# Kernel tuning notes

Measured on AMD Instinct MI355X. Metric: run time of the kernel, lower is better.

Reference implementation:

```python
import jax, jax.numpy as jnp
import numpy as np

B, L = 4, 2048
D_MODEL = 64          # d_model = input_size
ED = 128              # d_inner = expand_factor * d_model = hidden_size
N = 32                # d_state
DCONV = 16            # d_conv
NLAYERS = 4
DTRANK = 4            # ceil(d_model/16)
NCLS = 1
EPS = 1e-5


def setup_inputs() -> dict:
    key = jax.random.key(0)
    ks = jax.random.split(key, 10)
    g = lambda k, s, sc: jax.random.normal(k, s, dtype=jnp.float32) * sc
    inp = {}
    inp["x"] = jax.random.normal(ks[0], (B, L, D_MODEL), dtype=jnp.float32)
    inp["in_w"] = g(ks[1], (NLAYERS, 2 * ED, D_MODEL), 0.1)
    inp["in_b"] = jnp.zeros((NLAYERS, 2 * ED), jnp.float32)
    inp["conv_w"] = g(ks[2], (NLAYERS, ED, 1, DCONV), 0.1)  # depthwise kernel (OIH per group)
    inp["conv_b"] = jnp.zeros((NLAYERS, ED), jnp.float32)
    inp["xproj_w"] = g(ks[3], (NLAYERS, DTRANK + 2 * N, ED), 0.1)
    inp["dtproj_w"] = g(ks[4], (NLAYERS, ED, DTRANK), 0.5)
    inp["dtproj_b"] = g(ks[5], (NLAYERS, ED), 0.5)
    # S4D-real init: A[e, n] = n+1
    A = jnp.tile(jnp.arange(1, N + 1, dtype=jnp.float32), (ED, 1))
    inp["A_log"] = jnp.tile(jnp.log(A)[None], (NLAYERS, 1, 1))
    inp["Dp"] = jnp.ones((NLAYERS, ED), jnp.float32)
    inp["outproj_w"] = g(ks[6], (NLAYERS, D_MODEL, ED), 0.1)
    inp["outproj_b"] = jnp.zeros((NLAYERS, D_MODEL), jnp.float32)
    inp["norm_w"] = jnp.ones((NLAYERS, D_MODEL), jnp.float32)
    inp["fc_w"] = g(ks[7], (NCLS, ED), 0.1)
    inp["fc_b"] = jnp.zeros((NCLS,), jnp.float32)
    return inp


def _rmsnorm(x, w):
    return x * jax.lax.rsqrt(jnp.mean(x * x, axis=-1, keepdims=True) + EPS) * w


def _causal_dwconv(x, w, b):
    # x: [B,L,ED], w: [ED,1,DCONV] depthwise, causal left pad
    xt = jnp.swapaxes(x, 1, 2)  # [B,ED,L]
    y = jax.lax.conv_general_dilated(
        xt, w, window_strides=(1,), padding=[(DCONV - 1, 0)],
        dimension_numbers=("NCH", "OIH", "NCH"), feature_group_count=ED)
    return jnp.swapaxes(y, 1, 2) + b


def _mamba_block(h, in_w, in_b, conv_w, conv_b, xproj_w, dtproj_w, dtproj_b,
                 A_log, Dp, outproj_w, outproj_b, last):
    xz = jnp.einsum("bld,ed->ble", h, in_w) + in_b          # [B,L,2ED]
    xin, z = jnp.split(xz, 2, axis=-1)
    xc = jax.nn.silu(_causal_dwconv(xin, conv_w, conv_b))    # [B,L,ED]
    dbc = jnp.einsum("ble,re->blr", xc, xproj_w)             # [B,L,DTRANK+2N]
    delta = dbc[..., :DTRANK]
    Bm = dbc[..., DTRANK:DTRANK + N]                          # [B,L,N]
    Cm = dbc[..., DTRANK + N:]                                # [B,L,N]
    delta = jax.nn.softplus(jnp.einsum("blr,er->ble", delta, dtproj_w) + dtproj_b)
    A = -jnp.exp(A_log)                                       # [ED,N]
    dA = jnp.exp(delta[..., None] * A)                        # [B,L,ED,N]
    dBu = delta[..., None] * Bm[:, :, None, :] * xc[..., None]  # [B,L,ED,N]

    def step(hs, t):
        dA_t, dBu_t, C_t = t                                  # [B,ED,N],[B,ED,N],[B,N]
        hs = dA_t * hs + dBu_t
        y = jnp.einsum("ben,bn->be", hs, C_t)
        return hs, y

    h0 = jnp.zeros((xc.shape[0], ED, N), dtype=xc.dtype)
    _, ys = jax.lax.scan(step, h0, (jnp.swapaxes(dA, 0, 1),
                                    jnp.swapaxes(dBu, 0, 1),
                                    jnp.swapaxes(Cm, 0, 1)))
    y = jnp.swapaxes(ys, 0, 1) + Dp * xc                      # [B,L,ED]
    y = y * jax.nn.silu(z)
    if last:
        return y                                              # classifier taps d_inner features
    return jnp.einsum("ble,de->bld", y, outproj_w) + outproj_b


def reference(x, in_w, in_b, conv_w, conv_b, xproj_w, dtproj_w, dtproj_b,
              A_log, Dp, outproj_w, outproj_b, norm_w, fc_w, fc_b):
    h = x
    for i in range(NLAYERS - 1):
        h = h + _mamba_block(_rmsnorm(h, norm_w[i]), in_w[i], in_b[i], conv_w[i],
                             conv_b[i], xproj_w[i], dtproj_w[i], dtproj_b[i],
                             A_log[i], Dp[i], outproj_w[i], outproj_b[i], False)
    i = NLAYERS - 1
    y = _mamba_block(_rmsnorm(h, norm_w[i]), in_w[i], in_b[i], conv_w[i],
                     conv_b[i], xproj_w[i], dtproj_w[i], dtproj_b[i],
                     A_log[i], Dp[i], outproj_w[i], outproj_b[i], True)
    last_hidden = y[:, -1, :]                                 # [B,ED]
    return last_hidden @ fc_w.T + fc_b                        # [B,NCLS]
```

## Files before the change

### kernel.cpp

```cpp
#include <hip/hip_runtime.h>
#include <math.h>

#define BSZ 4
#define Lseq 2048
#define DM 64
#define ED 128
#define NST 32
#define DCONVK 16
#define NLAYERS 4
#define DTRANK 4
#define EPSV 1e-5f
#define NC 128
#define TT 16
#define NSEG 8
#define L2E 1.4426950408889634f

#if defined(__has_builtin)
#if __has_builtin(__builtin_amdgcn_exp2f)
#define EXP2F(x) __builtin_amdgcn_exp2f(x)
#else
#define EXP2F(x) exp2f(x)
#endif
#else
#define EXP2F(x) exp2f(x)
#endif

__device__ __forceinline__ float sigf(float x) { return 1.0f / (1.0f + __expf(-x)); }
__device__ __forceinline__ float hsum4(float4 a) { return (a.x + a.y) + (a.z + a.w); }

__device__ __forceinline__ void inproj16(
    const float* in_w_l, const float* in_b_l, const float (*hn)[DM],
    float* xin, float* zbuf, size_t t0, int tid)
{
    float4 w4[16];
    const float4* wr = (const float4*)(in_w_l + tid * DM);
    #pragma unroll
    for (int i = 0; i < 16; ++i) w4[i] = wr[i];
    const float bias = in_b_l[tid];
    #pragma unroll 2
    for (int tok = 0; tok < TT; ++tok) {
        const float4* hv4 = (const float4*)&hn[tok][0];
        float4 a4 = make_float4(0.f, 0.f, 0.f, 0.f);
        #pragma unroll
        for (int i = 0; i < 16; ++i) {
            float4 hv = hv4[i];
            a4.x = fmaf(hv.x, w4[i].x, a4.x);
            a4.y = fmaf(hv.y, w4[i].y, a4.y);
            a4.z = fmaf(hv.z, w4[i].z, a4.z);
            a4.w = fmaf(hv.w, w4[i].w, a4.w);
        }
        const float r = bias + hsum4(a4);
        if (tid < ED) xin[(t0 + tok) * ED + tid] = r;
        else          zbuf[(t0 + tok) * ED + (tid - ED)] = r;
    }
}

__global__ __launch_bounds__(256) void k_layer_gemm(
    const float* __restrict__ hin, const float* __restrict__ norm_w,
    const float* __restrict__ in_w, const float* __restrict__ in_b,
    float* __restrict__ xin, float* __restrict__ zb, float* __restrict__ out)
{
    const int t0 = blockIdx.x * TT;
    const int tid = threadIdx.x;
    const int lane = tid & 63;
    const int wv = tid >> 6;
    __shared__ __align__(16) float hn[TT][DM];

    if (blockIdx.x == 0 && tid < BSZ) out[tid] = 0.f;

    const float nw = norm_w[lane];
    float hval[4];
    #pragma unroll
    for (int j = 0; j < 4; ++j)
        hval[j] = hin[(size_t)(t0 + wv * 4 + j) * DM + lane];

    #pragma unroll
    for (int j = 0; j < 4; ++j) {
        float ss = hval[j] * hval[j];
        #pragma unroll
        for (int off = 32; off; off >>= 1) ss += __shfl_xor(ss, off, 64);
        const float sc = rsqrtf(ss * (1.0f / DM) + EPSV);
        hn[wv * 4 + j][lane] = hval[j] * sc * nw;
    }
    __syncthreads();
    inproj16(in_w, in_b, (const float (*)[DM])hn, xin, zb, (size_t)t0, tid);
}

__global__ __launch_bounds__(256) void k_conv_scan(
    const float* __restrict__ xin, const float* __restrict__ conv_w,
    const float* __restrict__ conv_b, const float* __restrict__ xproj_w,
    const float* __restrict__ dtproj_w, const float* __restrict__ dtproj_b,
    const float* __restrict__ A_log,
    float* __restrict__ xc_out, float* __restrict__ delta_out,
    float* __restrict__ Bout, float* __restrict__ Cout,
    float* __restrict__ dsum_out, float* __restrict__ hloc, int store_dbc)
{
    const int blk = blockIdx.x;
    const int b   = blk >> 7;
    const int c   = blk & 127;
    const int l0  = c * TT;
    const size_t t0 = (size_t)b * Lseq + l0;
    const int tid = threadIdx.x;
    const int e = tid & 127, half = tid >> 7;
    const bool doXC = store_dbc || (c == NC - 1);
    __shared__ __align__(16) float xs[(TT + DCONVK - 1) * ED];
    __shared__ __align__(16) float xcs[TT][ED];
    __shared__ __align__(16) float Bs[TT][NST];
    __shared__ float dts[TT][DTRANK];
    float (*dl)[ED] = (float (*)[ED])xs;

    float Aen16[16];
    {
        const float4* a4 = (const float4*)(A_log + e * NST + half * 16);
        #pragma unroll
        for (int i = 0; i < 4; ++i) {
            float4 v = a4[i];
            Aen16[i*4+0] = -__expf(v.x) * L2E; Aen16[i*4+1] = -__expf(v.y) * L2E;
            Aen16[i*4+2] = -__expf(v.z) * L2E; Aen16[i*4+3] = -__expf(v.w) * L2E;
        }
    }
    float w[DCONVK];
    {
        const float4* cw = (const float4*)(conv_w + e * DCONVK);
        #pragma unroll
        for (int i = 0; i < 4; ++i) {
            float4 cc = cw[i];
            w[i*4+0] = cc.x; w[i*4+1] = cc.y; w[i*4+2] = cc.z; w[i*4+3] = cc.w;
        }
    }
    const float cb = conv_b[e];

    {
        const int NV = (TT + DCONVK - 1) * ED / 4;
        for (int idx4 = tid; idx4 < NV; idx4 += 256) {
            const int row = idx4 >> 5;
            const int lrow = l0 - (DCONVK - 1) + row;
            float4 v = make_float4(0.f, 0.f, 0.f, 0.f);
            if (lrow >= 0)
                v = ((const float4*)(xin + ((size_t)b * Lseq + lrow) * ED))[idx4 & 31];
            ((float4*)xs)[idx4] = v;
        }
    }
    __syncthreads();

    {
        #pragma unroll 2
        for (int j = 0; j < 8; ++j) {
            const int tok = half * 8 + j;
            float acc = cb;
            #pragma unroll
            for (int k = 0; k < DCONVK; ++k)
                acc = fmaf(xs[(tok + k) * ED + e], w[k], acc);
            const float xcv = acc * sigf(acc);
            xcs[tok][e] = xcv;
            if (doXC) xc_out[(t0 + tok) * ED + e] = xcv;
        }
    }
    __syncthreads();

    {
        const int wv = tid >> 6, lane = tid & 63;
        float4 acc[4];
        #pragma unroll
        for (int j = 0; j < 4; ++j) acc[j] = make_float4(0.f, 0.f, 0.f, 0.f);
        #pragma unroll 1
        for (int p = 0; p < 4; ++p) {
            float4 w4[8];
            const float4* wr = (const float4*)(xproj_w + lane * ED + p * 32);
            #pragma unroll
            for (int i = 0; i < 8; ++i) w4[i] = wr[i];
            #pragma unroll
            for (int j = 0; j < 4; ++j) {
                const float4* yv = (const float4*)&xcs[wv * 4 + j][p * 32];
                #pragma unroll
                for (int i = 0; i < 8; ++i) {
                    float4 hv = yv[i];
                    acc[j].x = fmaf(hv.x, w4[i].x, acc[j].x);
                    acc[j].y = fmaf(hv.y, w4[i].y, acc[j].y);
                    acc[j].z = fmaf(hv.z, w4[i].z, acc[j].z);
                    acc[j].w = fmaf(hv.w, w4[i].w, acc[j].w);
                }
            }
        }
        #pragma unroll
        for (int j = 0; j < 4; ++j) {
            const int tok = wv * 4 + j;
            const float v = hsum4(acc[j]);
            if (lane < DTRANK) {
                dts[tok][lane] = v;
            } else if (lane < DTRANK + NST) {
                Bs[tok][lane - DTRANK] = v;
                if (store_dbc) Bout[(t0 + tok) * NST + (lane - DTRANK)] = v;
            } else {
                if (doXC) Cout[(t0 + tok) * NST + (lane - DTRANK - NST)] = v;
            }
        }
        {
            const int ridx = lane & 3;
            const int ks   = (lane >> 2) & 3;
            const int tsub = lane >> 4;
            const int r4   = 64 + ridx;
            const int tok  = wv * 4 + tsub;
            const float4* wr = (const float4*)(xproj_w + r4 * ED + ks * 32);
            const float4* yv = (const float4*)&xcs[tok][ks * 32];
            float4 a4 = make_float4(0.f, 0.f, 0.f, 0.f);
            #pragma unroll
            for (int i = 0; i < 8; ++i) {
                float4 hv = yv[i]; float4 wv4 = wr[i];
                a4.x = fmaf(hv.x, wv4.x, a4.x);
                a4.y = fmaf(hv.y, wv4.y, a4.y);
                a4.z = fmaf(hv.z, wv4.z, a4.z);
                a4.w = fmaf(hv.w, wv4.w, a4.w);
            }
            float v = hsum4(a4);
            v += __shfl_xor(v, 4, 64);
            v += __shfl_xor(v, 8, 64);
            if (ks == 0 && doXC) Cout[(t0 + tok) * NST + (r4 - DTRANK - NST)] = v;
        }
    }
    __syncthreads();

    {
        const float4 dwv = *(const float4*)(dtproj_w + e * DTRANK);
        const float bias = dtproj_b[e];
        #pragma unroll 2
        for (int j = 0; j < 8; ++j) {
            const int tok = half * 8 + j;
            float a = bias;
            a = fmaf(dts[tok][0], dwv.x, a);
            a = fmaf(dts[tok][1], dwv.y, a);
            a = fmaf(dts[tok][2], dwv.z, a);
            a = fmaf(dts[tok][3], dwv.w, a);
            const float sp = fmaxf(a, 0.f) + log1pf(__expf(-fabsf(a)));
            dl[tok][e] = sp;
            if (store_dbc) delta_out[(t0 + tok) * ED + e] = sp;
        }
    }
    __syncthreads();

    {
        float dsum = 0.f;
        #pragma unroll 4
        for (int l = 0; l < TT; ++l) dsum += dl[l][e];
        if (half == 0) dsum_out[((size_t)b * NC + c) * ED + e] = dsum;

        #pragma unroll 1
        for (int g = 0; g < 2; ++g) {
            const int n0 = half * 16 + g * 8;
            float Aen[8];
            #pragma unroll
            for (int k = 0; k < 8; ++k) Aen[k] = Aen16[g * 8 + k];
            float hs[8];
            #pragma unroll
            for (int k = 0; k < 8; ++k) hs[k] = 0.f;
            #pragma unroll 2
            for (int l = 0; l < TT; ++l) {
                const float de   = dl[l][e];
                const float dexc = de * xcs[l][e];
                const float4 B0 = *(const float4*)&Bs[l][n0];
                const float4 B1 = *(const float4*)&Bs[l][n0 + 4];
                float a;
                a = EXP2F(de * Aen[0]); hs[0] = fmaf(a, hs[0], B0.x * dexc);
                a = EXP2F(de * Aen[1]); hs[1] = fmaf(a, hs[1], B0.y * dexc);
                a = EXP2F(de * Aen[2]); hs[2] = fmaf(a, hs[2], B0.z * dexc);
                a = EXP2F(de * Aen[3]); hs[3] = fmaf(a, hs[3], B0.w * dexc);
                a = EXP2F(de * Aen[4]); hs[4] = fmaf(a, hs[4], B1.x * dexc);
                a = EXP2F(de * Aen[5]); hs[5] = fmaf(a, hs[5], B1.y * dexc);
                a = EXP2F(de * Aen[6]); hs[6] = fmaf(a, hs[6], B1.z * dexc);
                a = EXP2F(de * Aen[7]); hs[7] = fmaf(a, hs[7], B1.w * dexc);
            }
            const size_t idx = (((size_t)b * NC + c) * ED + e) * NST + n0;
            *(float4*)(hloc + idx)     = make_float4(hs[0], hs[1], hs[2], hs[3]);
            *(float4*)(hloc + idx + 4) = make_float4(hs[4], hs[5], hs[6], hs[7]);
        }
    }
}

__global__ __launch_bounds__(256) void k_scan_combine(
    const float* __restrict__ dsum, float* __restrict__ hloc,
    const float* __restrict__ A_log,
    const float* __restrict__ Cv, const float* __restrict__ xc,
    const float* __restrict__ zb, const float* __restrict__ Dp,
    const float* __restrict__ fcw, const float* __restrict__ fcb,
    float* __restrict__ out, int final)
{
    const int tid = threadIdx.x;
    const int tt  = tid & 31;
    const int seg = tid >> 5;
    const int t   = blockIdx.x * 32 + tt;
    const int b   = t >> 12;
    const int en  = t & 4095;
    const int e   = en >> 5;

    const float Aen2 = -__expf(A_log[en]) * L2E;

    const int c0 = seg * (NC / NSEG);
    const size_t idxBase = (size_t)b * NC * (ED * NST) + en;
    const size_t dBase   = (size_t)b * NC * ED + e;

    float u[NC / NSEG], a[NC / NSEG];
    #pragma unroll
    for (int k = 0; k < NC / NSEG; ++k)
        u[k] = hloc[idxBase + (size_t)(c0 + k) * (ED * NST)];
    #pragma unroll
    for (int k = 0; k < NC / NSEG; ++k)
        a[k] = EXP2F(Aen2 * dsum[dBase + (size_t)(c0 + k) * ED]);

    float A = 1.f, U = 0.f;
    #pragma unroll
    for (int k = 0; k < NC / NSEG; ++k) { U = fmaf(a[k], U, u[k]); A *= a[k]; }

    __shared__ float As[NSEG][32], Us[NSEG][32];
    As[seg][tt] = A; Us[seg][tt] = U;
    __syncthreads();

    float h = 0.f;
    #pragma unroll
    for (int j = 0; j < NSEG - 1; ++j)
        if (j < seg) h = fmaf(As[j][tt], h, Us[j][tt]);

    #pragma unroll
    for (int k = 0; k < NC / NSEG; ++k) {
        hloc[idxBase + (size_t)(c0 + k) * (ED * NST)] = h;
        h = fmaf(a[k], h, u[k]);
    }

    if (final && seg == NSEG - 1) {
        const int n = en & 31;
        const size_t tok = (size_t)b * Lseq + (Lseq - 1);
        float p = h * Cv[tok * NST + n];
        #pragma unroll
        for (int off = 16; off; off >>= 1) p += __shfl_xor(p, off, 32);
        if (n == 0) {
            const float xce = xc[tok * ED + e];
            const float zi  = zb[tok * ED + e];
            float val = (p + Dp[e] * xce) * (zi * sigf(zi)) * fcw[e];
            if (en == 0) val += fcb[0];
            atomicAdd(&out[b], val);
        }
    }
}

__global__ __launch_bounds__(256) void k_scan_gemm(
    const float* __restrict__ delta, const float* __restrict__ Bv,
    const float* __restrict__ Cv, const float* __restrict__ xc,
    const float* __restrict__ zbin, const float* __restrict__ A_log,
    const float* __restrict__ Dp, const float* __restrict__ hinit,
    const float* __restrict__ ow, const float* __restrict__ ob,
    const float* __restrict__ hin, const float* __restrict__ norm_w,
    const float* __restrict__ in_w, const float* __restrict__ in_b,
    float* __restrict__ hout, float* __restrict__ xin, float* __restrict__ zb)
{
    const int blk = blockIdx.x;
    const int b   = blk >> 7;
    const int c   = blk & 127;
    const int l0  = c * TT;
    const size_t t0 = (size_t)b * Lseq + l0;
    const int tid = threadIdx.x;
    const int e = tid & 127, half = tid >> 7;

    __shared__ __align__(16) float dlS[TT][ED];
    __shared__ __align__(16) float xcS[TT][ED];
    __shared__ __align__(16) float BsS[TT][NST];
    __shared__ __align__(16) float CsS[TT][NST];
    __shared__ __align__(16) float ys[TT][ED];
    __shared__ __align__(16) float pp[2][TT][ED];
    __shared__ __align__(16) float hn[TT][DM];

    float Aen16[16];
    {
        const float4* a4 = (const float4*)(A_log + e * NST + half * 16);
        #pragma unroll
        for (int i = 0; i < 4; ++i) {
            float4 v = a4[i];
            Aen16[i*4+0] = -__expf(v.x) * L2E; Aen16[i*4+1] = -__expf(v.y) * L2E;
            Aen16[i*4+2] = -__expf(v.z) * L2E; Aen16[i*4+3] = -__expf(v.w) * L2E;
        }
    }

    {
        const float4* dsrc = (const float4*)(delta + t0 * ED);
        const float4* xsrc = (const float4*)(xc + t0 * ED);
        float4* ddst = (float4*)&dlS[0][0];
        float4* xdst = (float4*)&xcS[0][0];
        #pragma unroll
        for (int i = 0; i < 2; ++i) {
            ddst[tid + i * 256] = dsrc[tid + i * 256];
            xdst[tid + i * 256] = xsrc[tid + i * 256];
        }
        if (tid < 128) {
            ((float4*)&BsS[0][0])[tid] = ((const float4*)(Bv + t0 * NST))[tid];
            ((float4*)&CsS[0][0])[tid] = ((const float4*)(Cv + t0 * NST))[tid];
        }
    }
    __syncthreads();

    #pragma unroll 1
    for (int g = 0; g < 2; ++g) {
        const int n0 = half * 16 + g * 8;
        float Aen[8];
        #pragma unroll
        for (int k = 0; k < 8; ++k) Aen[k] = Aen16[g * 8 + k];
        float hs[8];
        {
            const size_t idx = (((size_t)b * NC + c) * ED + e) * NST + n0;
            const float4 h0 = *(const float4*)(hinit + idx);
            const float4 h1 = *(const float4*)(hinit + idx + 4);
            hs[0] = h0.x; hs[1] = h0.y; hs[2] = h0.z; hs[3] = h0.w;
            hs[4] = h1.x; hs[5] = h1.y; hs[6] = h1.z; hs[7] = h1.w;
        }
        #pragma unroll 2
        for (int l = 0; l < TT; ++l) {
            const float de   = dlS[l][e];
            const float dexc = de * xcS[l][e];
            const float4 B0 = *(const float4*)&BsS[l][n0];
            const float4 B1 = *(const float4*)&BsS[l][n0 + 4];
            const float4 C0 = *(const float4*)&CsS[l][n0];
            const float4 C1 = *(const float4*)&CsS[l][n0 + 4];
            float a, p = 0.f;
            a = EXP2F(de * Aen[0]); hs[0] = fmaf(a, hs[0], B0.x * dexc); p = fmaf(hs[0], C0.x, p);
            a = EXP2F(de * Aen[1]); hs[1] = fmaf(a, hs[1], B0.y * dexc); p = fmaf(hs[1], C0.y, p);
            a = EXP2F(de * Aen[2]); hs[2] = fmaf(a, hs[2], B0.z * dexc); p = fmaf(hs[2], C0.z, p);
            a = EXP2F(de * Aen[3]); hs[3] = fmaf(a, hs[3], B0.w * dexc); p = fmaf(hs[3], C0.w, p);
            a = EXP2F(de * Aen[4]); hs[4] = fmaf(a, hs[4], B1.x * dexc); p = fmaf(hs[4], C1.x, p);
            a = EXP2F(de * Aen[5]); hs[5] = fmaf(a, hs[5], B1.y * dexc); p = fmaf(hs[5], C1.y, p);
            a = EXP2F(de * Aen[6]); hs[6] = fmaf(a, hs[6], B1.z * dexc); p = fmaf(hs[6], C1.z, p);
            a = EXP2F(de * Aen[7]); hs[7] = fmaf(a, hs[7], B1.w * dexc); p = fmaf(hs[7], C1.w, p);
            if (g == 0) pp[half][l][e] = p;
            else        pp[half][l][e] += p;
        }
    }
    __syncthreads();
    {
        const float dpe = Dp[e];
        #pragma unroll 2
        for (int j = 0; j < 8; ++j) {
            const int tl = half * 8 + j;
            const size_t tok = t0 + tl;
            const float p = pp[0][tl][e] + pp[1][tl][e];
            const float zi = zbin[tok * ED + e];
            ys[tl][e] = (p + dpe * xcS[tl][e]) * (zi * sigf(zi));
        }
    }
    __syncthreads();

    const int lane = tid & 63;
    const int wv = tid >> 6;
    const float nw = norm_w[lane];
    float hval[4];
    {
        float4 acc[4];
        #pragma unroll
        for (int j = 0; j < 4; ++j) acc[j] = make_float4(0.f, 0.f, 0.f, 0.f);
        #pragma unroll 1
        for (int p = 0; p < 4; ++p) {
            float4 w4[8];
            const float4* wr = (const float4*)(ow + lane * ED + p * 32);
            #pragma unroll
            for (int q = 0; q < 8; ++q) w4[q] = wr[q];
            #pragma unroll
            for (int j = 0; j < 4; ++j) {
                const float4* yv = (const float4*)&ys[wv * 4 + j][p * 32];
                #pragma unroll
                for (int q = 0; q < 8; ++q) {
                    float4 hv = yv[q];
                    acc[j].x = fmaf(hv.x, w4[q].x, acc[j].x);
                    acc[j].y = fmaf(hv.y, w4[q].y, acc[j].y);
                    acc[j].z = fmaf(hv.z, w4[q].z, acc[j].z);
                    acc[j].w = fmaf(hv.w, w4[q].w, acc[j].w);
                }
            }
        }
        const float obd = ob[lane];
        #pragma unroll
        for (int j = 0; j < 4; ++j) {
            const size_t tok = t0 + wv * 4 + j;
            hval[j] = hsum4(acc[j]) + obd + hin[tok * DM + lane];
            hout[tok * DM + lane] = hval[j];
        }
    }
    #pragma unroll
    for (int j = 0; j < 4; ++j) {
        float ss = hval[j] * hval[j];
        #pragma unroll
        for (int off = 32; off; off >>= 1) ss += __shfl_xor(ss, off, 64);
        const float sc = rsqrtf(ss * (1.0f / DM) + EPSV);
        hn[wv * 4 + j][lane] = hval[j] * sc * nw;
    }
    __syncthreads();
    inproj16(in_w, in_b, (const float (*)[DM])hn, xin, zb, t0, tid);
}

extern "C" void kernel_launch(void* const* d_in, const int* in_sizes, int n_in,
                              void* d_out, int out_size, void* d_ws, size_t ws_size,
                              hipStream_t stream)
{
    const float* x         = (const float*)d_in[0];
    const float* in_w      = (const float*)d_in[1];
    const float* in_b      = (const float*)d_in[2];
    const float* conv_w    = (const float*)d_in[3];
    const float* conv_b    = (const float*)d_in[4];
    const float* xproj_w   = (const float*)d_in[5];
    const float* dtproj_w  = (const float*)d_in[6];
    const float* dtproj_b  = (const float*)d_in[7];
    const float* A_log     = (const float*)d_in[8];
    const float* Dp        = (const float*)d_in[9];
    const float* outproj_w = (const float*)d_in[10];
    const float* outproj_b = (const float*)d_in[11];
    const float* norm_w    = (const float*)d_in[12];
    const float* fc_w      = (const float*)d_in[13];
    const float* fc_b      = (const float*)d_in[14];

    const size_t TOK = (size_t)BSZ * Lseq;
    float* ws = (float*)d_ws;
    float* h0    = ws; ws += TOK * DM;
    float* h1    = ws; ws += TOK * DM;
    float* xin   = ws; ws += TOK * ED;
    float* zbuf  = ws; ws += TOK * ED;
    float* xc    = ws; ws += TOK * ED;
    float* dlt   = ws; ws += TOK * ED;
    float* Bv    = ws; ws += TOK * NST;
    float* Cv    = ws; ws += TOK * NST;
    float* dsum  = ws; ws += (size_t)BSZ * NC * ED;
    float* hloc  = ws; ws += (size_t)BSZ * NC * ED * NST;

    const float* hres = x;
    float* hbufs[2] = { h0, h1 };

    k_layer_gemm<<<(int)(TOK / TT), 256, 0, stream>>>(
        x, norm_w, in_w, in_b, xin, zbuf, (float*)d_out);

    for (int i = 0; i < NLAYERS; ++i) {
        const int last = (i == NLAYERS - 1);
        const float* Alog_i = A_log + (size_t)i * ED * NST;
        k_conv_scan<<<(int)(BSZ * NC), 256, 0, stream>>>(
            xin, conv_w + (size_t)i * ED * DCONVK, conv_b + (size_t)i * ED,
            xproj_w + (size_t)i * (DTRANK + 2 * NST) * ED,
            dtproj_w + (size_t)i * ED * DTRANK, dtproj_b + (size_t)i * ED,
            Alog_i, xc, dlt, Bv, Cv, dsum, hloc, last ? 0 : 1);
        k_scan_combine<<<(BSZ * ED * NST * NSEG) / 256, 256, 0, stream>>>(
            dsum, hloc, Alog_i, Cv, xc, zbuf, Dp + (size_t)i * ED,
            fc_w, fc_b, (float*)d_out, last ? 1 : 0);
        if (!last) {
            float* hout = hbufs[i & 1];
            k_scan_gemm<<<(int)(BSZ * NC), 256, 0, stream>>>(
                dlt, Bv, Cv, xc, zbuf, Alog_i, Dp + (size_t)i * ED, hloc,
                outproj_w + (size_t)i * DM * ED, outproj_b + (size_t)i * DM,
                hres, norm_w + (size_t)(i + 1) * DM,
                in_w + (size_t)(i + 1) * 2 * ED * DM,
                in_b + (size_t)(i + 1) * 2 * ED,
                hout, xin, zbuf);
            hres = hout;
        }
    }
}
```

Before: 308.1 us.

## Fuse all layer kernels into one persistent kernel with grid barriers

```diff
diff --git a/kernel.cpp b/kernel.cpp
--- a/kernel.cpp
+++ b/kernel.cpp
@@ -13,6 +13,7 @@
 #define NC 128
 #define TT 16
 #define NSEG 8
+#define GRIDN (BSZ * NC)
 #define L2E 1.4426950408889634f
 
 #if defined(__has_builtin)
@@ -27,6 +28,19 @@
 
 __device__ __forceinline__ float sigf(float x) { return 1.0f / (1.0f + __expf(-x)); }
 __device__ __forceinline__ float hsum4(float4 a) { return (a.x + a.y) + (a.z + a.w); }
+
+__device__ __forceinline__ void gbar(unsigned int* cnt, unsigned int target)
+{
+    __syncthreads();
+    if (threadIdx.x == 0) {
+        __threadfence();
+        __hip_atomic_fetch_add(cnt, 1u, __ATOMIC_RELEASE, __HIP_MEMORY_SCOPE_AGENT);
+        while (__hip_atomic_load(cnt, __ATOMIC_RELAXED, __HIP_MEMORY_SCOPE_AGENT) < target)
+            __builtin_amdgcn_s_sleep(1);
+        __threadfence();
+    }
+    __syncthreads();
+}
 
 __device__ __forceinline__ void inproj16(
     const float* in_w_l, const float* in_b_l, const float (*hn)[DM],
@@ -55,462 +69,452 @@
     }
 }
 
-__global__ __launch_bounds__(256) void k_layer_gemm(
-    const float* __restrict__ hin, const float* __restrict__ norm_w,
-    const float* __restrict__ in_w, const float* __restrict__ in_b,
-    float* __restrict__ xin, float* __restrict__ zb, float* __restrict__ out)
+struct KParams {
+    const float *x, *in_w, *in_b, *conv_w, *conv_b, *xproj_w, *dtproj_w,
+                *dtproj_b, *A_log, *Dp, *outproj_w, *outproj_b, *norm_w,
+                *fc_w, *fc_b;
+    float *out, *h0, *h1, *xin, *zbuf, *xc, *dlt, *Bv, *Cv, *dsum, *hloc;
+    unsigned int* bar;
+};
+
+__global__ __launch_bounds__(256, 2) void k_mamba(KParams P)
 {
-    const int t0 = blockIdx.x * TT;
+    const int bid = blockIdx.x;
     const int tid = threadIdx.x;
-    const int lane = tid & 63;
-    const int wv = tid >> 6;
-    __shared__ __align__(16) float hn[TT][DM];
-
-    if (blockIdx.x == 0 && tid < BSZ) out[tid] = 0.f;
-
-    const float nw = norm_w[lane];
-    float hval[4];
-    #pragma unroll
-    for (int j = 0; j < 4; ++j)
-        hval[j] = hin[(size_t)(t0 + wv * 4 + j) * DM + lane];
-
-    #pragma unroll
-    for (int j = 0; j < 4; ++j) {
-        float ss = hval[j] * hval[j];
+    unsigned int bk = 0;
+    __shared__ __align__(16) float smem[12288];
+
+    if (bid == 0 && tid < BSZ) P.out[tid] = 0.f;
+
+    {
+        float (*hn)[DM] = (float (*)[DM])smem;
+        const size_t t0 = (size_t)bid * TT;
+        const int lane = tid & 63, wv = tid >> 6;
+        const float nw = P.norm_w[lane];
+        float hval[4];
         #pragma unroll
-        for (int off = 32; off; off >>= 1) ss += __shfl_xor(ss, off, 64);
-        const float sc = rsqrtf(ss * (1.0f / DM) + EPSV);
-        hn[wv * 4 + j][lane] = hval[j] * sc * nw;
+        for (int j = 0; j < 4; ++j)
+            hval[j] = P.x[(t0 + wv * 4 + j) * DM + lane];
+        #pragma unroll
+        for (int j = 0; j < 4; ++j) {
+            float ss = hval[j] * hval[j];
+            #pragma unroll
+            for (int off = 32; off; off >>= 1) ss += __shfl_xor(ss, off, 64);
+            const float sc = rsqrtf(ss * (1.0f / DM) + EPSV);
+            hn[wv * 4 + j][lane] = hval[j] * sc * nw;
+        }
+        __syncthreads();
+        inproj16(P.in_w, P.in_b, (const float (*)[DM])hn, P.xin, P.zbuf, t0, tid);
     }
-    __syncthreads();
-    inproj16(in_w, in_b, (const float (*)[DM])hn, xin, zb, (size_t)t0, tid);
-}
-
-__global__ __launch_bounds__(256) void k_conv_scan(
-    const float* __restrict__ xin, const float* __restrict__ conv_w,
-    const float* __restrict__ conv_b, const float* __restrict__ xproj_w,
-    const float* __restrict__ dtproj_w, const float* __restrict__ dtproj_b,
-    const float* __restrict__ A_log,
-    float* __restrict__ xc_out, float* __restrict__ delta_out,
-    float* __restrict__ Bout, float* __restrict__ Cout,
-    float* __restrict__ dsum_out, float* __restrict__ hloc, int store_dbc)
-{
-    const int blk = blockIdx.x;
-    const int b   = blk >> 7;
-    const int c   = blk & 127;
-    const int l0  = c * TT;
-    const size_t t0 = (size_t)b * Lseq + l0;
-    const int tid = threadIdx.x;
-    const int e = tid & 127, half = tid >> 7;
-    const bool doXC = store_dbc || (c == NC - 1);
-    __shared__ __align__(16) float xs[(TT + DCONVK - 1) * ED];
-    __shared__ __align__(16) float xcs[TT][ED];
-    __shared__ __align__(16) float Bs[TT][NST];
-    __shared__ float dts[TT][DTRANK];
-    float (*dl)[ED] = (float (*)[ED])xs;
-
-    float Aen16[16];
-    {
-        const float4* a4 = (const float4*)(A_log + e * NST + half * 16);
-        #pragma unroll
-        for (int i = 0; i < 4; ++i) {
-            float4 v = a4[i];
-            Aen16[i*4+0] = -__expf(v.x) * L2E; Aen16[i*4+1] = -__expf(v.y) * L2E;
-            Aen16[i*4+2] = -__expf(v.z) * L2E; Aen16[i*4+3] = -__expf(v.w) * L2E;
+    gbar(P.bar, ++bk * GRIDN);
+
+    #pragma unroll 1
+    for (int li = 0; li < NLAYERS; ++li) {
+        const int last = (li == NLAYERS - 1);
+        const float* Alog = P.A_log + (size_t)li * ED * NST;
+        const float* Dpl  = P.Dp + (size_t)li * ED;
+
+        {
+            const int b = bid >> 7, c = bid & 127;
+            const int l0 = c * TT;
+            const size_t t0 = (size_t)b * Lseq + l0;
+            const int e = tid & 127, half = tid >> 7;
+            const int store_dbc = last ? 0 : 1;
+            const bool doXC = store_dbc || (c == NC - 1);
+
+            float* xs = smem;
+            float (*xcs)[ED] = (float (*)[ED])(smem + 4096);
+            float (*Bs)[NST] = (float (*)[NST])(smem + 6144);
+            float (*dts)[DTRANK] = (float (*)[DTRANK])(smem + 6656);
+            float (*dl)[ED] = (float (*)[ED])xs;
+
+            const float* conv_w   = P.conv_w + (size_t)li * ED * DCONVK;
+            const float* conv_b   = P.conv_b + (size_t)li * ED;
+            const float* xproj_w  = P.xproj_w + (size_t)li * (DTRANK + 2 * NST) * ED;
+            const float* dtproj_w = P.dtproj_w + (size_t)li * ED * DTRANK;
+            const float* dtproj_b = P.dtproj_b + (size_t)li * ED;
+
+            float Aen16[16];
+            {
+                const float4* a4 = (const float4*)(Alog + e * NST + half * 16);
+                #pragma unroll
+                for (int i = 0; i < 4; ++i) {
+                    float4 v = a4[i];
+                    Aen16[i*4+0] = -__expf(v.x) * L2E; Aen16[i*4+1] = -__expf(v.y) * L2E;
+                    Aen16[i*4+2] = -__expf(v.z) * L2E; Aen16[i*4+3] = -__expf(v.w) * L2E;
+                }
+            }
+            float w[DCONVK];
+            {
+                const float4* cw = (const float4*)(conv_w + e * DCONVK);
+                #pragma unroll
+                for (int i = 0; i < 4; ++i) {
+                    float4 cc = cw[i];
+                    w[i*4+0] = cc.x; w[i*4+1] = cc.y; w[i*4+2] = cc.z; w[i*4+3] = cc.w;
+                }
+            }
+            const float cb = conv_b[e];
+
+            {
+                const int NV = (TT + DCONVK - 1) * ED / 4;
+                for (int idx4 = tid; idx4 < NV; idx4 += 256) {
+                    const int row = idx4 >> 5;
+                    const int lrow = l0 - (DCONVK - 1) + row;
+                    float4 v = make_float4(0.f, 0.f, 0.f, 0.f);
+                    if (lrow >= 0)
+                        v = ((const float4*)(P.xin + ((size_t)b * Lseq + lrow) * ED))[idx4 & 31];
+                    ((float4*)xs)[idx4] = v;
+                }
+            }
+            __syncthreads();
+
+            {
+                #pragma unroll 2
+                for (int j = 0; j < 8; ++j) {
+                    const int tok = half * 8 + j;
+                    float acc = cb;
+                    #pragma unroll
+                    for (int k = 0; k < DCONVK; ++k)
+                        acc = fmaf(xs[(tok + k) * ED + e], w[k], acc);
+                    const float xcv = acc * sigf(acc);
+                    xcs[tok][e] = xcv;
+                    if (doXC) P.xc[(t0 + tok) * ED + e] = xcv;
+                }
+            }
+            __syncthreads();
+
+            {
+                const int wv = tid >> 6, lane = tid & 63;
+                float4 acc[4];
+                #pragma unroll
+                for (int j = 0; j < 4; ++j) acc[j] = make_float4(0.f, 0.f, 0.f, 0.f);
+                #pragma unroll 1
+                for (int p = 0; p < 4; ++p) {
+                    float4 w4[8];
+                    const float4* wr = (const float4*)(xproj_w + lane * ED + p * 32);
+                    #pragma unroll
+                    for (int i = 0; i < 8; ++i) w4[i] = wr[i];
+                    #pragma unroll
+                    for (int j = 0; j < 4; ++j) {
+                        const float4* yv = (const float4*)&xcs[wv * 4 + j][p * 32];
+                        #pragma unroll
+                        for (int i = 0; i < 8; ++i) {
+                            float4 hv = yv[i];
+                            acc[j].x = fmaf(hv.x, w4[i].x, acc[j].x);
+                            acc[j].y = fmaf(hv.y, w4[i].y, acc[j].y);
+                            acc[j].z = fmaf(hv.z, w4[i].z, acc[j].z);
+                            acc[j].w = fmaf(hv.w, w4[i].w, acc[j].w);
+                        }
+                    }
+                }
+                #pragma unroll
+                for (int j = 0; j < 4; ++j) {
+                    const int tok = wv * 4 + j;
+                    const float v = hsum4(acc[j]);
+                    if (lane < DTRANK) {
+                        dts[tok][lane] = v;
+                    } else if (lane < DTRANK + NST) {
+                        Bs[tok][lane - DTRANK] = v;
+                        if (store_dbc) P.Bv[(t0 + tok) * NST + (lane - DTRANK)] = v;
+                    } else {
+                        if (doXC) P.Cv[(t0 + tok) * NST + (lane - DTRANK - NST)] = v;
+                    }
+                }
+                {
+                    const int ridx = lane & 3;
+                    const int ks   = (lane >> 2) & 3;
+                    const int tsub = lane >> 4;
+                    const int r4   = 64 + ridx;
+                    const int tok  = wv * 4 + tsub;
+                    const float4* wr = (const float4*)(xproj_w + r4 * ED + ks * 32);
+                    const float4* yv = (const float4*)&xcs[tok][ks * 32];
+                    float4 a4 = make_float4(0.f, 0.f, 0.f, 0.f);
+                    #pragma unroll
+                    for (int i = 0; i < 8; ++i) {
+                        float4 hv = yv[i]; float4 wv4 = wr[i];
+                        a4.x = fmaf(hv.x, wv4.x, a4.x);
+                        a4.y = fmaf(hv.y, wv4.y, a4.y);
+                        a4.z = fmaf(hv.z, wv4.z, a4.z);
+                        a4.w = fmaf(hv.w, wv4.w, a4.w);
+                    }
+                    float v = hsum4(a4);
+                    v += __shfl_xor(v, 4, 64);
+                    v += __shfl_xor(v, 8, 64);
+                    if (ks == 0 && doXC) P.Cv[(t0 + tok) * NST + (r4 - DTRANK - NST)] = v;
+                }
+            }
+            __syncthreads();
+
+            {
+                const float4 dwv = *(const float4*)(dtproj_w + e * DTRANK);
+                const float bias = dtproj_b[e];
+                #pragma unroll 2
+                for (int j = 0; j < 8; ++j) {
+                    const int tok = half * 8 + j;
+                    float a = bias;
+                    a = fmaf(dts[tok][0], dwv.x, a);
+                    a = fmaf(dts[tok][1], dwv.y, a);
+                    a = fmaf(dts[tok][2], dwv.z, a);
+                    a = fmaf(dts[tok][3], dwv.w, a);
+                    const float sp = fmaxf(a, 0.f) + log1pf(__expf(-fabsf(a)));
+                    dl[tok][e] = sp;
+                    if (store_dbc) P.dlt[(t0 + tok) * ED + e] = sp;
+                }
+            }
+            __syncthreads();
+
+            {
+                float dsum = 0.f;
+                #pragma unroll 4
+                for (int l = 0; l < TT; ++l) dsum += dl[l][e];
+                if (half == 0) P.dsum[((size_t)b * NC + c) * ED + e] = dsum;
+
+                #pragma unroll 1
+                for (int g = 0; g < 2; ++g) {
+                    const int n0 = half * 16 + g * 8;
+                    float Aen[8];
+                    #pragma unroll
+                    for (int k = 0; k < 8; ++k) Aen[k] = Aen16[g * 8 + k];
+                    float hs[8];
+                    #pragma unroll
+                    for (int k = 0; k < 8; ++k) hs[k] = 0.f;
+                    #pragma unroll 2
+                    for (int l = 0; l < TT; ++l) {
+                        const float de   = dl[l][e];
+                        const float dexc = de * xcs[l][e];
+                        const float4 B0 = *(const float4*)&Bs[l][n0];
+                        const float4 B1 = *(const float4*)&Bs[l][n0 + 4];
+                        float a;
+                        a = EXP2F(de * Aen[0]); hs[0] = fmaf(a, hs[0], B0.x * dexc);
+                        a = EXP2F(de * Aen[1]); hs[1] = fmaf(a, hs[1], B0.y * dexc);
+                        a = EXP2F(de * Aen[2]); hs[2] = fmaf(a, hs[2], B0.z * dexc);
+                        a = EXP2F(de * Aen[3]); hs[3] = fmaf(a, hs[3], B0.w * dexc);
+                        a = EXP2F(de * Aen[4]); hs[4] = fmaf(a, hs[4], B1.x * dexc);
+                        a = EXP2F(de * Aen[5]); hs[5] = fmaf(a, hs[5], B1.y * dexc);
+                        a = EXP2F(de * Aen[6]); hs[6] = fmaf(a, hs[6], B1.z * dexc);
+                        a = EXP2F(de * Aen[7]); hs[7] = fmaf(a, hs[7], B1.w * dexc);
+                    }
+                    const size_t idx = (((size_t)b * NC + c) * ED + e) * NST + n0;
+                    *(float4*)(P.hloc + idx)     = make_float4(hs[0], hs[1], hs[2], hs[3]);
+                    *(float4*)(P.hloc + idx + 4) = make_float4(hs[4], hs[5], hs[6], hs[7]);
+                }
+            }
+        }
+        gbar(P.bar, ++bk * GRIDN);
+
+        {
+            const int tt  = tid & 31;
+            const int seg = tid >> 5;
+            const int t   = bid * 32 + tt;
+            const int b   = t >> 12;
+            const int en  = t & 4095;
+            const int e   = en >> 5;
+
+            const float Aen2 = -__expf(Alog[en]) * L2E;
+
+            const int c0 = seg * (NC / NSEG);
+            const size_t idxBase = (size_t)b * NC * (ED * NST) + en;
+            const size_t dBase   = (size_t)b * NC * ED + e;
+
+            float u[NC / NSEG], a[NC / NSEG];
+            #pragma unroll
+            for (int k = 0; k < NC / NSEG; ++k)
+                u[k] = P.hloc[idxBase + (size_t)(c0 + k) * (ED * NST)];
+            #pragma unroll
+            for (int k = 0; k < NC / NSEG; ++k)
+                a[k] = EXP2F(Aen2 * P.dsum[dBase + (size_t)(c0 + k) * ED]);
+
+            float A = 1.f, U = 0.f;
+            #pragma unroll
+            for (int k = 0; k < NC / NSEG; ++k) { U = fmaf(a[k], U, u[k]); A *= a[k]; }
+
+            float (*As)[32] = (float (*)[32])smem;
+            float (*Us)[32] = (float (*)[32])(smem + NSEG * 32);
+            As[seg][tt] = A; Us[seg][tt] = U;
+            __syncthreads();
+
+            float h = 0.f;
+            #pragma unroll
+            for (int j = 0; j < NSEG - 1; ++j)
+                if (j < seg) h = fmaf(As[j][tt], h, Us[j][tt]);
+
+            #pragma unroll
+            for (int k = 0; k < NC / NSEG; ++k) {
+                P.hloc[idxBase + (size_t)(c0 + k) * (ED * NST)] = h;
+                h = fmaf(a[k], h, u[k]);
+            }
+
+            if (last && seg == NSEG - 1) {
+                const int n = en & 31;
+                const size_t tok = (size_t)b * Lseq + (Lseq - 1);
+                float p = h * P.Cv[tok * NST + n];
+                #pragma unroll
+                for (int off = 16; off; off >>= 1) p += __shfl_xor(p, off, 32);
+                if (n == 0) {
+                    const float xce = P.xc[tok * ED + e];
+                    const float zi  = P.zbuf[tok * ED + e];
+                    float val = (p + Dpl[e] * xce) * (zi * sigf(zi)) * P.fc_w[e];
+                    if (en == 0) val += P.fc_b[0];
+                    atomicAdd(&P.out[b], val);
+                }
+            }
+        }
+
+        if (!last) {
+            gbar(P.bar, ++bk * GRIDN);
+            {
+                const int b = bid >> 7, c = bid & 127;
+                const int l0 = c * TT;
+                const size_t t0 = (size_t)b * Lseq + l0;
+                const int e = tid & 127, half = tid >> 7;
+
+                float (*dlS)[ED] = (float (*)[ED])(smem);
+                float (*xcS)[ED] = (float (*)[ED])(smem + 2048);
+                float (*BsS)[NST] = (float (*)[NST])(smem + 4096);
+                float (*CsS)[NST] = (float (*)[NST])(smem + 4608);
+                float (*ys)[ED]  = (float (*)[ED])(smem + 5120);
+                float (*pp)[TT][ED] = (float (*)[TT][ED])(smem + 7168);
+                float (*hn)[DM]  = (float (*)[DM])(smem + 11264);
+
+                const float* ow = P.outproj_w + (size_t)li * DM * ED;
+                const float* ob = P.outproj_b + (size_t)li * DM;
+                const float* hres = (li == 0) ? P.x : ((li == 1) ? P.h0 : P.h1);
+                float* hout = (li & 1) ? P.h1 : P.h0;
+
+                float Aen16[16];
+                {
+                    const float4* a4 = (const float4*)(Alog + e * NST + half * 16);
+                    #pragma unroll
+                    for (int i = 0; i < 4; ++i) {
+                        float4 v = a4[i];
+                        Aen16[i*4+0] = -__expf(v.x) * L2E; Aen16[i*4+1] = -__expf(v.y) * L2E;
+                        Aen16[i*4+2] = -__expf(v.z) * L2E; Aen16[i*4+3] = -__expf(v.w) * L2E;
+                    }
+                }
+
+                {
+                    const float4* dsrc = (const float4*)(P.dlt + t0 * ED);
+                    const float4* xsrc = (const float4*)(P.xc + t0 * ED);
+                    float4* ddst = (float4*)&dlS[0][0];
+                    float4* xdst = (float4*)&xcS[0][0];
+                    #pragma unroll
+                    for (int i = 0; i < 2; ++i) {
+                        ddst[tid + i * 256] = dsrc[tid + i * 256];
+                        xdst[tid + i * 256] = xsrc[tid + i * 256];
+                    }
+                    if (tid < 128) {
+                        ((float4*)&BsS[0][0])[tid] = ((const float4*)(P.Bv + t0 * NST))[tid];
+                        ((float4*)&CsS[0][0])[tid] = ((const float4*)(P.Cv + t0 * NST))[tid];
+                    }
+                }
+                __syncthreads();
+
+                #pragma unroll 1
+                for (int g = 0; g < 2; ++g) {
+                    const int n0 = half * 16 + g * 8;
+                    float Aen[8];
+                    #pragma unroll
+                    for (int k = 0; k < 8; ++k) Aen[k] = Aen16[g * 8 + k];
+                    float hs[8];
+                    {
+                        const size_t idx = (((size_t)b * NC + c) * ED + e) * NST + n0;
+                        const float4 h0v = *(const float4*)(P.hloc + idx);
+                        const float4 h1v = *(const float4*)(P.hloc + idx + 4);
+                        hs[0] = h0v.x; hs[1] = h0v.y; hs[2] = h0v.z; hs[3] = h0v.w;
+                        hs[4] = h1v.x; hs[5] = h1v.y; hs[6] = h1v.z; hs[7] = h1v.w;
+                    }
+                    #pragma unroll 2
+                    for (int l = 0; l < TT; ++l) {
+                        const float de   = dlS[l][e];
+                        const float dexc = de * xcS[l][e];
+                        const float4 B0 = *(const float4*)&BsS[l][n0];
+                        const float4 B1 = *(const float4*)&BsS[l][n0 + 4];
+                        const float4 C0 = *(const float4*)&CsS[l][n0];
+                        const float4 C1 = *(const float4*)&CsS[l][n0 + 4];
+                        float a, p = 0.f;
+                        a = EXP2F(de * Aen[0]); hs[0] = fmaf(a, hs[0], B0.x * dexc); p = fmaf(hs[0], C0.x, p);
+                        a = EXP2F(de * Aen[1]); hs[1] = fmaf(a, hs[1], B0.y * dexc); p = fmaf(hs[1], C0.y, p);
+                        a = EXP2F(de * Aen[2]); hs[2] = fmaf(a, hs[2], B0.z * dexc); p = fmaf(hs[2], C0.z, p);
+                        a = EXP2F(de * Aen[3]); hs[3] = fmaf(a, hs[3], B0.w * dexc); p = fmaf(hs[3], C0.w, p);
+                        a = EXP2F(de * Aen[4]); hs[4] = fmaf(a, hs[4], B1.x * dexc); p = fmaf(hs[4], C1.x, p);
+                        a = EXP2F(de * Aen[5]); hs[5] = fmaf(a, hs[5], B1.y * dexc); p = fmaf(hs[5], C1.y, p);
+                        a = EXP2F(de * Aen[6]); hs[6] = fmaf(a, hs[6], B1.z * dexc); p = fmaf(hs[6], C1.z, p);
+                        a = EXP2F(de * Aen[7]); hs[7] = fmaf(a, hs[7], B1.w * dexc); p = fmaf(hs[7], C1.w, p);
+                        if (g == 0) pp[half][l][e] = p;
+                        else        pp[half][l][e] += p;
+                    }
+                }
+                __syncthreads();
+                {
+                    const float dpe = Dpl[e];
+                    #pragma unroll 2
+                    for (int j = 0; j < 8; ++j) {
+                        const int tl = half * 8 + j;
+                        const size_t tok = t0 + tl;
+                        const float p = pp[0][tl][e] + pp[1][tl][e];
+                        const float zi = P.zbuf[tok * ED + e];
+                        ys[tl][e] = (p + dpe * xcS[tl][e]) * (zi * sigf(zi));
+                    }
+                }
+                __syncthreads();
+
+                const int lane = tid & 63;
+                const int wv = tid >> 6;
+                const float nw = P.norm_w[(size_t)(li + 1) * DM + lane];
+                float hval[4];
+                {
+                    float4 acc[4];
+                    #pragma unroll
+                    for (int j = 0; j < 4; ++j) acc[j] = make_float4(0.f, 0.f, 0.f, 0.f);
+                    #pragma unroll 1
+                    for (int p = 0; p < 4; ++p) {
+                        float4 w4[8];
+                        const float4* wr = (const float4*)(ow + lane * ED + p * 32);
+                        #pragma unroll
+                        for (int q = 0; q < 8; ++q) w4[q] = wr[q];
+                        #pragma unroll
+                        for (int j = 0; j < 4; ++j) {
+                            const float4* yv = (const float4*)&ys[wv * 4 + j][p * 32];
+                            #pragma unroll
+                            for (int q = 0; q < 8; ++q) {
+                                float4 hv = yv[q];
+                                acc[j].x = fmaf(hv.x, w4[q].x, acc[j].x);
+                                acc[j].y = fmaf(hv.y, w4[q].y, acc[j].y);
+                                acc[j].z = fmaf(hv.z, w4[q].z, acc[j].z);
+                                acc[j].w = fmaf(hv.w, w4[q].w, acc[j].w);
+                            }
+                        }
+                    }
+                    const float obd = ob[lane];
+                    #pragma unroll
+                    for (int j = 0; j < 4; ++j) {
+                        const size_t tok = t0 + wv * 4 + j;
+                        hval[j] = hsum4(acc[j]) + obd + hres[tok * DM + lane];
+                        hout[tok * DM + lane] = hval[j];
+                    }
+                }
+                #pragma unroll
+                for (int j = 0; j < 4; ++j) {
+                    float ss = hval[j] * hval[j];
+                    #pragma unroll
+                    for (int off = 32; off; off >>= 1) ss += __shfl_xor(ss, off, 64);
+                    const float sc = rsqrtf(ss * (1.0f / DM) + EPSV);
+                    hn[wv * 4 + j][lane] = hval[j] * sc * nw;
+                }
+                __syncthreads();
+                inproj16(P.in_w + (size_t)(li + 1) * 2 * ED * DM,
+                         P.in_b + (size_t)(li + 1) * 2 * ED,
+                         (const float (*)[DM])hn, P.xin, P.zbuf, t0, tid);
+            }
+            gbar(P.bar, ++bk * GRIDN);
         }
     }
-    float w[DCONVK];
-    {
-        const float4* cw = (const float4*)(conv_w + e * DCONVK);
-        #pragma unroll
-        for (int i = 0; i < 4; ++i) {
-            float4 cc = cw[i];
-            w[i*4+0] = cc.x; w[i*4+1] = cc.y; w[i*4+2] = cc.z; w[i*4+3] = cc.w;
-        }
-    }
-    const float cb = conv_b[e];
-
-    {
-        const int NV = (TT + DCONVK - 1) * ED / 4;
-        for (int idx4 = tid; idx4 < NV; idx4 += 256) {
-            const int row = idx4 >> 5;
-            const int lrow = l0 - (DCONVK - 1) + row;
-            float4 v = make_float4(0.f, 0.f, 0.f, 0.f);
-            if (lrow >= 0)
-                v = ((const float4*)(xin + ((size_t)b * Lseq + lrow) * ED))[idx4 & 31];
-            ((float4*)xs)[idx4] = v;
-        }
-    }
-    __syncthreads();
-
-    {
-        #pragma unroll 2
-        for (int j = 0; j < 8; ++j) {
-            const int tok = half * 8 + j;
-            float acc = cb;
-            #pragma unroll
-            for (int k = 0; k < DCONVK; ++k)
-                acc = fmaf(xs[(tok + k) * ED + e], w[k], acc);
-            const float xcv = acc * sigf(acc);
-            xcs[tok][e] = xcv;
-            if (doXC) xc_out[(t0 + tok) * ED + e] = xcv;
-        }
-    }
-    __syncthreads();
-
-    {
-        const int wv = tid >> 6, lane = tid & 63;
-        float4 acc[4];
-        #pragma unroll
-        for (int j = 0; j < 4; ++j) acc[j] = make_float4(0.f, 0.f, 0.f, 0.f);
-        #pragma unroll 1
-        for (int p = 0; p < 4; ++p) {
-            float4 w4[8];
-            const float4* wr = (const float4*)(xproj_w + lane * ED + p * 32);
-            #pragma unroll
-            for (int i = 0; i < 8; ++i) w4[i] = wr[i];
-            #pragma unroll
-            for (int j = 0; j < 4; ++j) {
-                const float4* yv = (const float4*)&xcs[wv * 4 + j][p * 32];
-                #pragma unroll
-                for (int i = 0; i < 8; ++i) {
-                    float4 hv = yv[i];
-                    acc[j].x = fmaf(hv.x, w4[i].x, acc[j].x);
-                    acc[j].y = fmaf(hv.y, w4[i].y, acc[j].y);
-                    acc[j].z = fmaf(hv.z, w4[i].z, acc[j].z);
-                    acc[j].w = fmaf(hv.w, w4[i].w, acc[j].w);
-                }
-            }
-        }
-        #pragma unroll
-        for (int j = 0; j < 4; ++j) {
-            const int tok = wv * 4 + j;
-            const float v = hsum4(acc[j]);
-            if (lane < DTRANK) {
-                dts[tok][lane] = v;
-            } else if (lane < DTRANK + NST) {
-                Bs[tok][lane - DTRANK] = v;
-                if (store_dbc) Bout[(t0 + tok) * NST + (lane - DTRANK)] = v;
-            } else {
-                if (doXC) Cout[(t0 + tok) * NST + (lane - DTRANK - NST)] = v;
-            }
-        }
-        {
-            const int ridx = lane & 3;
-            const int ks   = (lane >> 2) & 3;
-            const int tsub = lane >> 4;
-            const int r4   = 64 + ridx;
-            const int tok  = wv * 4 + tsub;
-            const float4* wr = (const float4*)(xproj_w + r4 * ED + ks * 32);
-            const float4* yv = (const float4*)&xcs[tok][ks * 32];
-            float4 a4 = make_float4(0.f, 0.f, 0.f, 0.f);
-            #pragma unroll
-            for (int i = 0; i < 8; ++i) {
-                float4 hv = yv[i]; float4 wv4 = wr[i];
-                a4.x = fmaf(hv.x, wv4.x, a4.x);
-                a4.y = fmaf(hv.y, wv4.y, a4.y);
-                a4.z = fmaf(hv.z, wv4.z, a4.z);
-                a4.w = fmaf(hv.w, wv4.w, a4.w);
-            }
-            float v = hsum4(a4);
-            v += __shfl_xor(v, 4, 64);
-            v += __shfl_xor(v, 8, 64);
-            if (ks == 0 && doXC) Cout[(t0 + tok) * NST + (r4 - DTRANK - NST)] = v;
-        }
-    }
-    __syncthreads();
-
-    {
-        const float4 dwv = *(const float4*)(dtproj_w + e * DTRANK);
-        const float bias = dtproj_b[e];
-        #pragma unroll 2
-        for (int j = 0; j < 8; ++j) {
-            const int tok = half * 8 + j;
-            float a = bias;
-            a = fmaf(dts[tok][0], dwv.x, a);
-            a = fmaf(dts[tok][1], dwv.y, a);
-            a = fmaf(dts[tok][2], dwv.z, a);
-            a = fmaf(dts[tok][3], dwv.w, a);
-            const float sp = fmaxf(a, 0.f) + log1pf(__expf(-fabsf(a)));
-            dl[tok][e] = sp;
-            if (store_dbc) delta_out[(t0 + tok) * ED + e] = sp;
-        }
-    }
-    __syncthreads();
-
-    {
-        float dsum = 0.f;
-        #pragma unroll 4
-        for (int l = 0; l < TT; ++l) dsum += dl[l][e];
-        if (half == 0) dsum_out[((size_t)b * NC + c) * ED + e] = dsum;
-
-        #pragma unroll 1
-        for (int g = 0; g < 2; ++g) {
-            const int n0 = half * 16 + g * 8;
-            float Aen[8];
-            #pragma unroll
-            for (int k = 0; k < 8; ++k) Aen[k] = Aen16[g * 8 + k];
-            float hs[8];
-            #pragma unroll
-            for (int k = 0; k < 8; ++k) hs[k] = 0.f;
-            #pragma unroll 2
-            for (int l = 0; l < TT; ++l) {
-                const float de   = dl[l][e];
-                const float dexc = de * xcs[l][e];
-                const float4 B0 = *(const float4*)&Bs[l][n0];
-                const float4 B1 = *(const float4*)&Bs[l][n0 + 4];
-                float a;
-                a = EXP2F(de * Aen[0]); hs[0] = fmaf(a, hs[0], B0.x * dexc);
-                a = EXP2F(de * Aen[1]); hs[1] = fmaf(a, hs[1], B0.y * dexc);
-                a = EXP2F(de * Aen[2]); hs[2] = fmaf(a, hs[2], B0.z * dexc);
-                a = EXP2F(de * Aen[3]); hs[3] = fmaf(a, hs[3], B0.w * dexc);
-                a = EXP2F(de * Aen[4]); hs[4] = fmaf(a, hs[4], B1.x * dexc);
-                a = EXP2F(de * Aen[5]); hs[5] = fmaf(a, hs[5], B1.y * dexc);
-                a = EXP2F(de * Aen[6]); hs[6] = fmaf(a, hs[6], B1.z * dexc);
-                a = EXP2F(de * Aen[7]); hs[7] = fmaf(a, hs[7], B1.w * dexc);
-            }
-            const size_t idx = (((size_t)b * NC + c) * ED + e) * NST + n0;
-            *(float4*)(hloc + idx)     = make_float4(hs[0], hs[1], hs[2], hs[3]);
-            *(float4*)(hloc + idx + 4) = make_float4(hs[4], hs[5], hs[6], hs[7]);
-        }
-    }
-}
-
-__global__ __launch_bounds__(256) void k_scan_combine(
-    const float* __restrict__ dsum, float* __restrict__ hloc,
-    const float* __restrict__ A_log,
-    const float* __restrict__ Cv, const float* __restrict__ xc,
-    const float* __restrict__ zb, const float* __restrict__ Dp,
-    const float* __restrict__ fcw, const float* __restrict__ fcb,
-    float* __restrict__ out, int final)
-{
-    const int tid = threadIdx.x;
-    const int tt  = tid & 31;
-    const int seg = tid >> 5;
-    const int t   = blockIdx.x * 32 + tt;
-    const int b   = t >> 12;
-    const int en  = t & 4095;
-    const int e   = en >> 5;
-
-    const float Aen2 = -__expf(A_log[en]) * L2E;
-
-    const int c0 = seg * (NC / NSEG);
-    const size_t idxBase = (size_t)b * NC * (ED * NST) + en;
-    const size_t dBase   = (size_t)b * NC * ED + e;
-
-    float u[NC / NSEG], a[NC / NSEG];
-    #pragma unroll
-    for (int k = 0; k < NC / NSEG; ++k)
-        u[k] = hloc[idxBase + (size_t)(c0 + k) * (ED * NST)];
-    #pragma unroll
-    for (int k = 0; k < NC / NSEG; ++k)
-        a[k] = EXP2F(Aen2 * dsum[dBase + (size_t)(c0 + k) * ED]);
-
-    float A = 1.f, U = 0.f;
-    #pragma unroll
-    for (int k = 0; k < NC / NSEG; ++k) { U = fmaf(a[k], U, u[k]); A *= a[k]; }
-
-    __shared__ float As[NSEG][32], Us[NSEG][32];
-    As[seg][tt] = A; Us[seg][tt] = U;
-    __syncthreads();
-
-    float h = 0.f;
-    #pragma unroll
-    for (int j = 0; j < NSEG - 1; ++j)
-        if (j < seg) h = fmaf(As[j][tt], h, Us[j][tt]);
-
-    #pragma unroll
-    for (int k = 0; k < NC / NSEG; ++k) {
-        hloc[idxBase + (size_t)(c0 + k) * (ED * NST)] = h;
-        h = fmaf(a[k], h, u[k]);
-    }
-
-    if (final && seg == NSEG - 1) {
-        const int n = en & 31;
-        const size_t tok = (size_t)b * Lseq + (Lseq - 1);
-        float p = h * Cv[tok * NST + n];
-        #pragma unroll
-        for (int off = 16; off; off >>= 1) p += __shfl_xor(p, off, 32);
-        if (n == 0) {
-            const float xce = xc[tok * ED + e];
-            const float zi  = zb[tok * ED + e];
-            float val = (p + Dp[e] * xce) * (zi * sigf(zi)) * fcw[e];
-            if (en == 0) val += fcb[0];
-            atomicAdd(&out[b], val);
-        }
-    }
-}
-
-__global__ __launch_bounds__(256) void k_scan_gemm(
-    const float* __restrict__ delta, const float* __restrict__ Bv,
-    const float* __restrict__ Cv, const float* __restrict__ xc,
-    const float* __restrict__ zbin, const float* __restrict__ A_log,
-    const float* __restrict__ Dp, const float* __restrict__ hinit,
-    const float* __restrict__ ow, const float* __restrict__ ob,
-    const float* __restrict__ hin, const float* __restrict__ norm_w,
-    const float* __restrict__ in_w, const float* __restrict__ in_b,
-    float* __restrict__ hout, float* __restrict__ xin, float* __restrict__ zb)
-{
-    const int blk = blockIdx.x;
-    const int b   = blk >> 7;
-    const int c   = blk & 127;
-    const int l0  = c * TT;
-    const size_t t0 = (size_t)b * Lseq + l0;
-    const int tid = threadIdx.x;
-    const int e = tid & 127, half = tid >> 7;
-
-    __shared__ __align__(16) float dlS[TT][ED];
-    __shared__ __align__(16) float xcS[TT][ED];
-    __shared__ __align__(16) float BsS[TT][NST];
-    __shared__ __align__(16) float CsS[TT][NST];
-    __shared__ __align__(16) float ys[TT][ED];
-    __shared__ __align__(16) float pp[2][TT][ED];
-    __shared__ __align__(16) float hn[TT][DM];
-
-    float Aen16[16];
-    {
-        const float4* a4 = (const float4*)(A_log + e * NST + half * 16);
-        #pragma unroll
-        for (int i = 0; i < 4; ++i) {
-            float4 v = a4[i];
-            Aen16[i*4+0] = -__expf(v.x) * L2E; Aen16[i*4+1] = -__expf(v.y) * L2E;
-            Aen16[i*4+2] = -__expf(v.z) * L2E; Aen16[i*4+3] = -__expf(v.w) * L2E;
-        }
-    }
-
-    {
-        const float4* dsrc = (const float4*)(delta + t0 * ED);
-        const float4* xsrc = (const float4*)(xc + t0 * ED);
-        float4* ddst = (float4*)&dlS[0][0];
-        float4* xdst = (float4*)&xcS[0][0];
-        #pragma unroll
-        for (int i = 0; i < 2; ++i) {
-            ddst[tid + i * 256] = dsrc[tid + i * 256];
-            xdst[tid + i * 256] = xsrc[tid + i * 256];
-        }
-        if (tid < 128) {
-            ((float4*)&BsS[0][0])[tid] = ((const float4*)(Bv + t0 * NST))[tid];
-            ((float4*)&CsS[0][0])[tid] = ((const float4*)(Cv + t0 * NST))[tid];
-        }
-    }
-    __syncthreads();
-
-    #pragma unroll 1
-    for (int g = 0; g < 2; ++g) {
-        const int n0 = half * 16 + g * 8;
-        float Aen[8];
-        #pragma unroll
-        for (int k = 0; k < 8; ++k) Aen[k] = Aen16[g * 8 + k];
-        float hs[8];
-        {
-            const size_t idx = (((size_t)b * NC + c) * ED + e) * NST + n0;
-            const float4 h0 = *(const float4*)(hinit + idx);
-            const float4 h1 = *(const float4*)(hinit + idx + 4);
-            hs[0] = h0.x; hs[1] = h0.y; hs[2] = h0.z; hs[3] = h0.w;
-            hs[4] = h1.x; hs[5] = h1.y; hs[6] = h1.z; hs[7] = h1.w;
-        }
-        #pragma unroll 2
-        for (int l = 0; l < TT; ++l) {
-            const float de   = dlS[l][e];
-            const float dexc = de * xcS[l][e];
-            const float4 B0 = *(const float4*)&BsS[l][n0];
-            const float4 B1 = *(const float4*)&BsS[l][n0 + 4];
-            const float4 C0 = *(const float4*)&CsS[l][n0];
-            const float4 C1 = *(const float4*)&CsS[l][n0 + 4];
-            float a, p = 0.f;
-            a = EXP2F(de * Aen[0]); hs[0] = fmaf(a, hs[0], B0.x * dexc); p = fmaf(hs[0], C0.x, p);
-            a = EXP2F(de * Aen[1]); hs[1] = fmaf(a, hs[1], B0.y * dexc); p = fmaf(hs[1], C0.y, p);
-            a = EXP2F(de * Aen[2]); hs[2] = fmaf(a, hs[2], B0.z * dexc); p = fmaf(hs[2], C0.z, p);
-            a = EXP2F(de * Aen[3]); hs[3] = fmaf(a, hs[3], B0.w * dexc); p = fmaf(hs[3], C0.w, p);
-            a = EXP2F(de * Aen[4]); hs[4] = fmaf(a, hs[4], B1.x * dexc); p = fmaf(hs[4], C1.x, p);
-            a = EXP2F(de * Aen[5]); hs[5] = fmaf(a, hs[5], B1.y * dexc); p = fmaf(hs[5], C1.y, p);
-            a = EXP2F(de * Aen[6]); hs[6] = fmaf(a, hs[6], B1.z * dexc); p = fmaf(hs[6], C1.z, p);
-            a = EXP2F(de * Aen[7]); hs[7] = fmaf(a, hs[7], B1.w * dexc); p = fmaf(hs[7], C1.w, p);
-            if (g == 0) pp[half][l][e] = p;
-            else        pp[half][l][e] += p;
-        }
-    }
-    __syncthreads();
-    {
-        const float dpe = Dp[e];
-        #pragma unroll 2
-        for (int j = 0; j < 8; ++j) {
-            const int tl = half * 8 + j;
-            const size_t tok = t0 + tl;
-            const float p = pp[0][tl][e] + pp[1][tl][e];
-            const float zi = zbin[tok * ED + e];
-            ys[tl][e] = (p + dpe * xcS[tl][e]) * (zi * sigf(zi));
-        }
-    }
-    __syncthreads();
-
-    const int lane = tid & 63;
-    const int wv = tid >> 6;
-    const float nw = norm_w[lane];
-    float hval[4];
-    {
-        float4 acc[4];
-        #pragma unroll
-        for (int j = 0; j < 4; ++j) acc[j] = make_float4(0.f, 0.f, 0.f, 0.f);
-        #pragma unroll 1
-        for (int p = 0; p < 4; ++p) {
-            float4 w4[8];
-            const float4* wr = (const float4*)(ow + lane * ED + p * 32);
-            #pragma unroll
-            for (int q = 0; q < 8; ++q) w4[q] = wr[q];
-            #pragma unroll
-            for (int j = 0; j < 4; ++j) {
-                const float4* yv = (const float4*)&ys[wv * 4 + j][p * 32];
-                #pragma unroll
-                for (int q = 0; q < 8; ++q) {
-                    float4 hv = yv[q];
-                    acc[j].x = fmaf(hv.x, w4[q].x, acc[j].x);
-                    acc[j].y = fmaf(hv.y, w4[q].y, acc[j].y);
-                    acc[j].z = fmaf(hv.z, w4[q].z, acc[j].z);
-                    acc[j].w = fmaf(hv.w, w4[q].w, acc[j].w);
-                }
-            }
-        }
-        const float obd = ob[lane];
-        #pragma unroll
-        for (int j = 0; j < 4; ++j) {
-            const size_t tok = t0 + wv * 4 + j;
-            hval[j] = hsum4(acc[j]) + obd + hin[tok * DM + lane];
-            hout[tok * DM + lane] = hval[j];
-        }
-    }
-    #pragma unroll
-    for (int j = 0; j < 4; ++j) {
-        float ss = hval[j] * hval[j];
-        #pragma unroll
-        for (int off = 32; off; off >>= 1) ss += __shfl_xor(ss, off, 64);
-        const float sc = rsqrtf(ss * (1.0f / DM) + EPSV);
-        hn[wv * 4 + j][lane] = hval[j] * sc * nw;
-    }
-    __syncthreads();
-    inproj16(in_w, in_b, (const float (*)[DM])hn, xin, zb, t0, tid);
 }
 
 extern "C" void kernel_launch(void* const* d_in, const int* in_sizes, int n_in,
                               void* d_out, int out_size, void* d_ws, size_t ws_size,
                               hipStream_t stream)
 {
-    const float* x         = (const float*)d_in[0];
-    const float* in_w      = (const float*)d_in[1];
-    const float* in_b      = (const float*)d_in[2];
-    const float* conv_w    = (const float*)d_in[3];
-    const float* conv_b    = (const float*)d_in[4];
-    const float* xproj_w   = (const float*)d_in[5];
-    const float* dtproj_w  = (const float*)d_in[6];
-    const float* dtproj_b  = (const float*)d_in[7];
-    const float* A_log     = (const float*)d_in[8];
-    const float* Dp        = (const float*)d_in[9];
-    const float* outproj_w = (const float*)d_in[10];
-    const float* outproj_b = (const float*)d_in[11];
-    const float* norm_w    = (const float*)d_in[12];
-    const float* fc_w      = (const float*)d_in[13];
-    const float* fc_b      = (const float*)d_in[14];
-
     const size_t TOK = (size_t)BSZ * Lseq;
     float* ws = (float*)d_ws;
     float* h0    = ws; ws += TOK * DM;
@@ -523,34 +527,29 @@
     float* Cv    = ws; ws += TOK * NST;
     float* dsum  = ws; ws += (size_t)BSZ * NC * ED;
     float* hloc  = ws; ws += (size_t)BSZ * NC * ED * NST;
-
-    const float* hres = x;
-    float* hbufs[2] = { h0, h1 };
-
-    k_layer_gemm<<<(int)(TOK / TT), 256, 0, stream>>>(
-        x, norm_w, in_w, in_b, xin, zbuf, (float*)d_out);
-
-    for (int i = 0; i < NLAYERS; ++i) {
-        const int last = (i == NLAYERS - 1);
-        const float* Alog_i = A_log + (size_t)i * ED * NST;
-        k_conv_scan<<<(int)(BSZ * NC), 256, 0, stream>>>(
-            xin, conv_w + (size_t)i * ED * DCONVK, conv_b + (size_t)i * ED,
-            xproj_w + (size_t)i * (DTRANK + 2 * NST) * ED,
-            dtproj_w + (size_t)i * ED * DTRANK, dtproj_b + (size_t)i * ED,
-            Alog_i, xc, dlt, Bv, Cv, dsum, hloc, last ? 0 : 1);
-        k_scan_combine<<<(BSZ * ED * NST * NSEG) / 256, 256, 0, stream>>>(
-            dsum, hloc, Alog_i, Cv, xc, zbuf, Dp + (size_t)i * ED,
-            fc_w, fc_b, (float*)d_out, last ? 1 : 0);
-        if (!last) {
-            float* hout = hbufs[i & 1];
-            k_scan_gemm<<<(int)(BSZ * NC), 256, 0, stream>>>(
-                dlt, Bv, Cv, xc, zbuf, Alog_i, Dp + (size_t)i * ED, hloc,
-                outproj_w + (size_t)i * DM * ED, outproj_b + (size_t)i * DM,
-                hres, norm_w + (size_t)(i + 1) * DM,
-                in_w + (size_t)(i + 1) * 2 * ED * DM,
-                in_b + (size_t)(i + 1) * 2 * ED,
-                hout, xin, zbuf);
-            hres = hout;
-        }
-    }
+    unsigned int* bar = (unsigned int*)ws; ws += 64;
+
+    KParams prm;
+    prm.x         = (const float*)d_in[0];
+    prm.in_w      = (const float*)d_in[1];
+    prm.in_b      = (const float*)d_in[2];
+    prm.conv_w    = (const float*)d_in[3];
+    prm.conv_b    = (const float*)d_in[4];
+    prm.xproj_w   = (const float*)d_in[5];
+    prm.dtproj_w  = (const float*)d_in[6];
+    prm.dtproj_b  = (const float*)d_in[7];
+    prm.A_log     = (const float*)d_in[8];
+    prm.Dp        = (const float*)d_in[9];
+    prm.outproj_w = (const float*)d_in[10];
+    prm.outproj_b = (const float*)d_in[11];
+    prm.norm_w    = (const float*)d_in[12];
+    prm.fc_w      = (const float*)d_in[13];
+    prm.fc_b      = (const float*)d_in[14];
+    prm.out  = (float*)d_out;
+    prm.h0 = h0; prm.h1 = h1; prm.xin = xin; prm.zbuf = zbuf;
+    prm.xc = xc; prm.dlt = dlt; prm.Bv = Bv; prm.Cv = Cv;
+    prm.dsum = dsum; prm.hloc = hloc; prm.bar = bar;
+
+    hipMemsetAsync(bar, 0, 256, stream);
+    k_mamba<<<dim3(GRIDN), dim3(256), 0, stream>>>(prm);
 }
```

Result: slower. 983.3 us (+219.2%).
